# Kernel optimization log

Measured on AMD Instinct MI355X. Metric: run time of the kernel, lower is better.

## Reference

```python
import jax, jax.numpy as jnp
import numpy as np

B, N, H, IN, D, ET = 16, 128, 256, 4, 2, 2
E = N * (N - 1)
NRF = 4 * D + 1            # num_relative_features = 9 (2D)
NODE_F = IN + NRF + D      # 15
EDGE_F = 2 * NRF + IN + D  # 24
EPS = 1e-8


def _norm(v):
    return jnp.sqrt(jnp.sum(v * v, axis=-1, keepdims=True) + EPS)


def _rot(R, v):
    return jnp.einsum('...ij,...j->...i', R, v)


def _relfeat(dp, dv, R, dth):
    # rotation-invariant relative features in frame R: rotated rel pos/vel,
    # distances, polar angles, heading difference -> 2+2+1+1+1+1+1 = 9 dims
    rp = _rot(R, dp)
    rv = _rot(R, dv)
    ang = jnp.arctan2(rp[..., 1:2], rp[..., 0:1])
    vang = jnp.arctan2(rv[..., 1:2], rv[..., 0:1])
    return jnp.concatenate([rp, rv, _norm(dp), ang, _norm(dv), vang, dth], -1)


def _forward(inputs, hidden, edges, predicted_field,
             msg_fc1_w, msg_fc1_b, msg_fc2_w, msg_fc2_b,
             pm_fc1_w, pm_fc1_b, pm_fc2_w, pm_fc2_b,
             hidden_r_w, hidden_i_w, hidden_h_w,
             present_r_w, present_r_b, present_i_w, present_i_b,
             present_n_w, present_n_b,
             input_r_w, input_r_b, input_i_w, input_i_b, input_n_w, input_n_b,
             out_w1, out_b1, out_w2, out_b2, out_w3, out_b3,
             send, recv):
    # ---- recurrent message passing on hidden state ----
    pre_msg = jnp.concatenate([hidden[:, recv], hidden[:, send]], -1)  # [B,E,2H]
    all_msgs = jnp.zeros((B, E, H), pre_msg.dtype)
    for i in range(1, ET):  # skip_first_edge_type = True
        m = jnp.tanh(pre_msg @ msg_fc1_w[i].T + msg_fc1_b[i])
        m = jnp.tanh(m @ msg_fc2_w[i].T + msg_fc2_b[i])
        all_msgs = all_msgs + m * edges[:, :, i:i + 1]
    agg_msgs = jnp.zeros((B, N, H), all_msgs.dtype).at[:, recv].add(all_msgs) / (N - 1)

    # ---- localizer: per-node frame from velocity heading ----
    ext = jnp.concatenate([inputs, predicted_field], -1)  # [B,N,6]
    pos, vel, field = ext[..., :D], ext[..., D:2 * D], ext[..., 2 * D:]
    theta = jnp.arctan2(vel[..., 1], vel[..., 0])  # [B,N]
    c, s = jnp.cos(theta), jnp.sin(theta)
    R = jnp.stack([jnp.stack([c, s], -1), jnp.stack([-s, c], -1)], -2)  # [B,N,2,2]
    Rinv = jnp.swapaxes(R, -1, -2)

    loc_pos, loc_vel, loc_field = _rot(R, pos), _rot(R, vel), _rot(R, field)
    rel_self = _relfeat(pos, vel, R, theta[..., None])
    rel_feat = jnp.concatenate([rel_self, loc_pos, loc_vel, loc_field], -1)  # [B,N,15]

    dp = pos[:, send] - pos[:, recv]
    dv = vel[:, send] - vel[:, recv]
    dth = (theta[:, send] - theta[:, recv])[..., None]
    f1 = _relfeat(dp, dv, R[:, recv], dth)
    f2 = _relfeat(-dp, -dv, R[:, send], -dth)
    edge_attr = jnp.concatenate(
        [f1, f2, loc_pos[:, recv], loc_vel[:, recv], loc_field[:, recv]], -1)  # [B,E,24]

    # ---- present (observation) message passing ----
    present_msgs = jnp.zeros((B, E, H), edge_attr.dtype)
    for i in range(1, ET):
        m = jax.nn.relu(edge_attr @ pm_fc1_w[i].T + pm_fc1_b[i])
        m = jax.nn.relu(m @ pm_fc2_w[i].T + pm_fc2_b[i])
        present_msgs = present_msgs + m * edges[:, :, i:i + 1]
    present_agg = jnp.zeros((B, N, H), present_msgs.dtype).at[:, recv].add(present_msgs) / (N - 1)

    # ---- GRU-style gated update ----
    inp_r = rel_feat @ input_r_w.T + input_r_b + present_agg @ present_r_w.T + present_r_b
    inp_i = rel_feat @ input_i_w.T + input_i_b + present_agg @ present_i_w.T + present_i_b
    inp_n = rel_feat @ input_n_w.T + input_n_b + present_agg @ present_n_w.T + present_n_b
    r = jax.nn.sigmoid(inp_r + agg_msgs @ hidden_r_w.T)
    i_g = jax.nn.sigmoid(inp_i + agg_msgs @ hidden_i_w.T)
    n_g = jnp.tanh(inp_n + r * (agg_msgs @ hidden_h_w.T))
    hidden_new = (1.0 - i_g) * n_g + i_g * hidden

    # ---- output MLP + globalizer ----
    h1 = jax.nn.relu(hidden_new @ out_w1.T + out_b1)
    h2 = jax.nn.relu(h1 @ out_w2.T + out_b2)
    pred = h2 @ out_w3.T + out_b3  # [B,N,4]
    pred_global = jnp.concatenate(
        [_rot(Rinv, pred[..., :D]), _rot(Rinv, pred[..., D:2 * D])], -1)
    outputs = inputs + pred_global
    return outputs, hidden_new


def setup_inputs():
    key = jax.random.key(0)
    ks = iter(jax.random.split(key, 48))
    rn = lambda *s: jax.random.normal(next(ks), s, jnp.float32)
    w = lambda *s: rn(*s) * 0.05
    send, recv = np.where(~np.eye(N, dtype=bool))
    return dict(
        inputs=rn(B, N, IN), hidden=rn(B, N, H),
        edges=jax.random.uniform(next(ks), (B, E, ET), jnp.float32),
        predicted_field=rn(B, N, D),
        msg_fc1_w=w(ET, H, 2 * H), msg_fc1_b=w(ET, H),
        msg_fc2_w=w(ET, H, H), msg_fc2_b=w(ET, H),
        pm_fc1_w=w(ET, H, EDGE_F), pm_fc1_b=w(ET, H),
        pm_fc2_w=w(ET, H, H), pm_fc2_b=w(ET, H),
        hidden_r_w=w(H, H), hidden_i_w=w(H, H), hidden_h_w=w(H, H),
        present_r_w=w(H, H), present_r_b=w(H),
        present_i_w=w(H, H), present_i_b=w(H),
        present_n_w=w(H, H), present_n_b=w(H),
        input_r_w=w(H, NODE_F), input_r_b=w(H),
        input_i_w=w(H, NODE_F), input_i_b=w(H),
        input_n_w=w(H, NODE_F), input_n_b=w(H),
        out_w1=w(H, H), out_b1=w(H), out_w2=w(H, H), out_b2=w(H),
        out_w3=w(IN, H), out_b3=w(IN),
        send_edges=jnp.asarray(send, jnp.int32),
        recv_edges=jnp.asarray(recv, jnp.int32),
    )


def reference(inputs, hidden, edges, predicted_field,
              msg_fc1_w, msg_fc1_b, msg_fc2_w, msg_fc2_b,
              pm_fc1_w, pm_fc1_b, pm_fc2_w, pm_fc2_b,
              hidden_r_w, hidden_i_w, hidden_h_w,
              present_r_w, present_r_b, present_i_w, present_i_b,
              present_n_w, present_n_b,
              input_r_w, input_r_b, input_i_w, input_i_b, input_n_w, input_n_b,
              out_w1, out_b1, out_w2, out_b2, out_w3, out_b3,
              send_edges, recv_edges):
    return _forward(inputs, hidden, edges, predicted_field,
                    msg_fc1_w, msg_fc1_b, msg_fc2_w, msg_fc2_b,
                    pm_fc1_w, pm_fc1_b, pm_fc2_w, pm_fc2_b,
                    hidden_r_w, hidden_i_w, hidden_h_w,
                    present_r_w, present_r_b, present_i_w, present_i_b,
                    present_n_w, present_n_b,
                    input_r_w, input_r_b, input_i_w, input_i_b, input_n_w, input_n_b,
                    out_w1, out_b1, out_w2, out_b2, out_w3, out_b3,
                    send_edges, recv_edges)
```

## Files before the change

### kernel.cpp

```cpp
#include <hip/hip_runtime.h>
#include <math.h>

#define BB 16
#define NN 128
#define HH 256
#define EE (NN*(NN-1))

typedef unsigned short ushort_t;
typedef __attribute__((ext_vector_type(8))) short bf16x8;
typedef __attribute__((ext_vector_type(4))) float f32x4;

__device__ __forceinline__ ushort_t f2b(float f) {
  unsigned u = __builtin_bit_cast(unsigned, f);
  unsigned r = (u + 0x7fffu + ((u >> 16) & 1u)) >> 16;
  return (ushort_t)r;
}

__device__ __forceinline__ float fast_tanh(float x) {
  float xx = fminf(fmaxf(x, -15.f), 15.f);
  float e = __builtin_amdgcn_exp2f(xx * 2.8853900817779268f);
  return (e - 1.f) * __builtin_amdgcn_rcpf(e + 1.f);
}
__device__ __forceinline__ float fast_sigmoid(float x) {
  float xx = fminf(fmaxf(x, -30.f), 30.f);
  float e = __builtin_amdgcn_exp2f(-xx * 1.4426950408889634f);
  return __builtin_amdgcn_rcpf(1.f + e);
}

__global__ void k_node_geom(const float* __restrict__ inputs,
                            const float* __restrict__ pfield,
                            float* __restrict__ geom, float* __restrict__ relf) {
  int idx = blockIdx.x * blockDim.x + threadIdx.x;
  if (idx >= BB * NN) return;
  float px = inputs[idx*4+0], py = inputs[idx*4+1];
  float vx = inputs[idx*4+2], vy = inputs[idx*4+3];
  float fx = pfield[idx*2+0], fy = pfield[idx*2+1];
  float th = atan2f(vy, vx);
  float c = cosf(th), s = sinf(th);
  float lpx =  c*px + s*py, lpy = -s*px + c*py;
  float lvx =  c*vx + s*vy, lvy = -s*vx + c*vy;
  float lfx =  c*fx + s*fy, lfy = -s*fx + c*fy;
  float np_ = sqrtf(px*px + py*py + 1e-8f);
  float nv_ = sqrtf(vx*vx + vy*vy + 1e-8f);
  float ang  = atan2f(lpy, lpx);
  float vang = atan2f(lvy, lvx);
  float* g = geom + idx*16;
  g[0]=px; g[1]=py; g[2]=vx; g[3]=vy; g[4]=th; g[5]=c; g[6]=s;
  g[7]=lpx; g[8]=lpy; g[9]=lvx; g[10]=lvy; g[11]=lfx; g[12]=lfy;
  float* r = relf + idx*16;
  r[0]=lpx; r[1]=lpy; r[2]=lvx; r[3]=lvy; r[4]=np_; r[5]=ang; r[6]=nv_; r[7]=vang; r[8]=th;
  r[9]=lpx; r[10]=lpy; r[11]=lvx; r[12]=lvy; r[13]=lfx; r[14]=lfy;
}

__global__ void k_cvt(const float* __restrict__ w2, const float* __restrict__ pw2,
                      ushort_t* __restrict__ w2b, ushort_t* __restrict__ pw2b) {
  int idx = blockIdx.x * 256 + threadIdx.x;
  if (idx < HH*HH) w2b[idx] = f2b(w2[HH*HH + idx]);
  else { int k = idx - HH*HH; pw2b[k] = f2b(pw2[HH*HH + k]); }
}

__global__ __launch_bounds__(256) void k_hab(const float* __restrict__ hidden,
                                             const float* __restrict__ w1,
                                             const float* __restrict__ b1,
                                             float* __restrict__ Ha,
                                             float* __restrict__ Hb) {
  int n = blockIdx.x >> 1, half = blockIdx.x & 1;
  int tid = threadIdx.x;
  __shared__ float x[8][HH];
  for (int q = 0; q < 8; ++q) {
    int b = half*8 + q;
    x[q][tid] = hidden[(b*NN + n)*HH + tid];
  }
  __syncthreads();
  const float* wa = w1 + (HH*2*HH) + tid*(2*HH);
  const float* wb = wa + HH;
  float accA[8], accB[8];
  float bias = b1[HH + tid];
  #pragma unroll
  for (int q = 0; q < 8; ++q) { accA[q] = bias; accB[q] = 0.f; }
  for (int k = 0; k < HH; k += 4) {
    float4 a4 = *(const float4*)(wa + k);
    float4 b4 = *(const float4*)(wb + k);
    #pragma unroll
    for (int q = 0; q < 8; ++q) {
      float4 x4 = *(const float4*)(&x[q][k]);
      accA[q] += x4.x*a4.x + x4.y*a4.y + x4.z*a4.z + x4.w*a4.w;
      accB[q] += x4.x*b4.x + x4.y*b4.y + x4.z*b4.z + x4.w*b4.w;
    }
  }
  for (int q = 0; q < 8; ++q) {
    int b = half*8 + q;
    Ha[(b*NN + n)*HH + tid] = accA[q];
    Hb[(b*NN + n)*HH + tid] = accB[q];
  }
}

__global__ __launch_bounds__(256, 4) void k_edge(
    const float* __restrict__ Ha, const float* __restrict__ Hb,
    const float* __restrict__ geom, const float* __restrict__ edges,
    const ushort_t* __restrict__ w2b, const float* __restrict__ b2,
    const ushort_t* __restrict__ pw2b, const float* __restrict__ pb2,
    const float* __restrict__ pw1, const float* __restrict__ pb1,
    float* __restrict__ agg0, float* __restrict__ agg1,
    float* __restrict__ pagg0, float* __restrict__ pagg1) {
  int half = blockIdx.x & 1;
  int j = (blockIdx.x >> 1) & 127;
  int b = blockIdx.x >> 8;
  int tid = threadIdx.x;
  int lane = tid & 63;
  int wv = tid >> 6;
  int lrow = lane & 15, lk = lane >> 4;

  __shared__ __align__(16) unsigned char m1s[64*512];
  __shared__ float attrS[64][24];
  __shared__ float HajS[HH];
  __shared__ float wgtS[64];
  __shared__ float gjS[13];

  HajS[tid] = Ha[(b*NN + j)*HH + tid];
  if (tid < 13) gjS[tid] = geom[(b*NN + j)*16 + tid];
  __syncthreads();

  if (tid < 64) {
    int il = tid;
    int i = half*64 + il;
    const float* gi = geom + (b*NN + i)*16;
    float dpx = gi[0]-gjS[0], dpy = gi[1]-gjS[1];
    float dvx = gi[2]-gjS[2], dvy = gi[3]-gjS[3];
    float dth = gi[4]-gjS[4];
    float cj = gjS[5], sj = gjS[6];
    float ci = gi[5],  si = gi[6];
    float ndp = sqrtf(dpx*dpx + dpy*dpy + 1e-8f);
    float ndv = sqrtf(dvx*dvx + dvy*dvy + 1e-8f);
    float r1x =  cj*dpx + sj*dpy, r1y = -sj*dpx + cj*dpy;
    float v1x =  cj*dvx + sj*dvy, v1y = -sj*dvx + cj*dvy;
    attrS[il][0]=r1x; attrS[il][1]=r1y; attrS[il][2]=v1x; attrS[il][3]=v1y;
    attrS[il][4]=ndp; attrS[il][5]=atan2f(r1y, r1x);
    attrS[il][6]=ndv; attrS[il][7]=atan2f(v1y, v1x); attrS[il][8]=dth;
    float r2x = -(ci*dpx + si*dpy), r2y = si*dpx - ci*dpy;
    float v2x = -(ci*dvx + si*dvy), v2y = si*dvx - ci*dvy;
    attrS[il][9]=r2x; attrS[il][10]=r2y; attrS[il][11]=v2x; attrS[il][12]=v2y;
    attrS[il][13]=ndp; attrS[il][14]=atan2f(r2y, r2x);
    attrS[il][15]=ndv; attrS[il][16]=atan2f(v2y, v2x); attrS[il][17]=-dth;
    attrS[il][18]=gjS[7]; attrS[il][19]=gjS[8]; attrS[il][20]=gjS[9];
    attrS[il][21]=gjS[10]; attrS[il][22]=gjS[11]; attrS[il][23]=gjS[12];
    float w = 0.f;
    if (i != j) {
      int e = i*127 + (j < i ? j : j-1);
      w = edges[(b*EE + e)*2 + 1];
    }
    wgtS[il] = w;
  }

  {
    float haj = HajS[tid];
    const float* hb = Hb + (b*NN + half*64)*HH + tid;
    #pragma unroll
    for (int i0 = 0; i0 < 64; i0 += 8) {
      float v[8];
      #pragma unroll
      for (int u = 0; u < 8; ++u) v[u] = hb[(i0+u)*HH];
      #pragma unroll
      for (int u = 0; u < 8; ++u) {
        int row = i0 + u;
        *(ushort_t*)(m1s + row*512 + ((tid*2) ^ ((row&15)<<4))) =
            f2b(fast_tanh(haj + v[u]));
      }
    }
  }
  __syncthreads();

  f32x4 zero = {0.f, 0.f, 0.f, 0.f};

  {
    f32x4 acc[4][4];
    #pragma unroll
    for (int rt = 0; rt < 4; ++rt)
      #pragma unroll
      for (int nt = 0; nt < 4; ++nt) acc[rt][nt] = zero;
    for (int kk = 0; kk < 8; ++kk) {
      bf16x8 afr[4];
      #pragma unroll
      for (int rt = 0; rt < 4; ++rt) {
        int row = rt*16 + lrow;
        afr[rt] = *reinterpret_cast<const bf16x8*>(
            m1s + row*512 + ((kk*64 + lk*16) ^ ((row&15)<<4)));
      }
      #pragma unroll
      for (int nt = 0; nt < 4; ++nt) {
        int col = wv*64 + nt*16 + lrow;
        bf16x8 bfr = *reinterpret_cast<const bf16x8*>(w2b + col*HH + kk*32 + lk*8);
        #pragma unroll
        for (int rt = 0; rt < 4; ++rt)
          acc[rt][nt] = __builtin_amdgcn_mfma_f32_16x16x32_bf16(afr[rt], bfr, acc[rt][nt], 0, 0, 0);
      }
    }
    float* aggOut = half ? agg1 : agg0;
    #pragma unroll
    for (int nt = 0; nt < 4; ++nt) {
      int col = wv*64 + nt*16 + lrow;
      float bias = b2[col];
      float p = 0.f;
      #pragma unroll
      for (int rt = 0; rt < 4; ++rt)
        #pragma unroll
        for (int r = 0; r < 4; ++r) {
          int row = rt*16 + lk*4 + r;
          p += fast_tanh(acc[rt][nt][r] + bias) * wgtS[row];
        }
      p += __shfl_xor(p, 16);
      p += __shfl_xor(p, 32);
      if (lane < 16)
        aggOut[(b*NN + j)*HH + wv*64 + nt*16 + lane] = p * (1.0f/127.0f);
    }
  }
  __syncthreads();

  {
    float wrow[24];
    #pragma unroll
    for (int k = 0; k < 24; ++k) wrow[k] = pw1[tid*24 + k];
    float bias = pb1[tid];
    #pragma unroll 2
    for (int i = 0; i < 64; ++i) {
      float s = bias;
      #pragma unroll
      for (int k = 0; k < 24; k += 4) {
        float4 a4 = *(const float4*)(&attrS[i][k]);
        s += a4.x*wrow[k] + a4.y*wrow[k+1] + a4.z*wrow[k+2] + a4.w*wrow[k+3];
      }
      s = fmaxf(s, 0.f);
      *(ushort_t*)(m1s + i*512 + ((tid*2) ^ ((i&15)<<4))) = f2b(s);
    }
  }
  __syncthreads();

  {
    f32x4 acc[4][4];
    #pragma unroll
    for (int rt = 0; rt < 4; ++rt)
      #pragma unroll
      for (int nt = 0; nt < 4; ++nt) acc[rt][nt] = zero;
    for (int kk = 0; kk < 8; ++kk) {
      bf16x8 afr[4];
      #pragma unroll
      for (int rt = 0; rt < 4; ++rt) {
        int row = rt*16 + lrow;
        afr[rt] = *reinterpret_cast<const bf16x8*>(
            m1s + row*512 + ((kk*64 + lk*16) ^ ((row&15)<<4)));
      }
      #pragma unroll
      for (int nt = 0; nt < 4; ++nt) {
        int col = wv*64 + nt*16 + lrow;
        bf16x8 bfr = *reinterpret_cast<const bf16x8*>(pw2b + col*HH + kk*32 + lk*8);
        #pragma unroll
        for (int rt = 0; rt < 4; ++rt)
          acc[rt][nt] = __builtin_amdgcn_mfma_f32_16x16x32_bf16(afr[rt], bfr, acc[rt][nt], 0, 0, 0);
      }
    }
    float* paggOut = half ? pagg1 : pagg0;
    #pragma unroll
    for (int nt = 0; nt < 4; ++nt) {
      int col = wv*64 + nt*16 + lrow;
      float bias = pb2[col];
      float p = 0.f;
      #pragma unroll
      for (int rt = 0; rt < 4; ++rt)
        #pragma unroll
        for (int r = 0; r < 4; ++r) {
          int row = rt*16 + lk*4 + r;
          p += fmaxf(acc[rt][nt][r] + bias, 0.f) * wgtS[row];
        }
      p += __shfl_xor(p, 16);
      p += __shfl_xor(p, 32);
      if (lane < 16)
        paggOut[(b*NN + j)*HH + wv*64 + nt*16 + lane] = p * (1.0f/127.0f);
    }
  }
}

__global__ __launch_bounds__(256) void k_gru(
    const float* __restrict__ inputs, const float* __restrict__ hidden,
    const float* __restrict__ geom, const float* __restrict__ relf,
    const float* __restrict__ agg0, const float* __restrict__ agg1,
    const float* __restrict__ pagg0, const float* __restrict__ pagg1,
    const float* __restrict__ hr_w, const float* __restrict__ hi_w, const float* __restrict__ hh_w,
    const float* __restrict__ pr_w, const float* __restrict__ pr_b,
    const float* __restrict__ pi_w, const float* __restrict__ pi_b,
    const float* __restrict__ pn_w, const float* __restrict__ pn_b,
    const float* __restrict__ ir_w, const float* __restrict__ ir_b,
    const float* __restrict__ ii_w, const float* __restrict__ ii_b,
    const float* __restrict__ in_w, const float* __restrict__ in_b,
    const float* __restrict__ ow1, const float* __restrict__ ob1,
    const float* __restrict__ ow2, const float* __restrict__ ob2,
    const float* __restrict__ ow3, const float* __restrict__ ob3,
    float* __restrict__ out_o, float* __restrict__ out_h) {
  int n = blockIdx.x >> 1, half = blockIdx.x & 1;
  int tid = threadIdx.x;
  __shared__ float paS[8][HH], agS[8][HH], hS[8][HH], t0S[8][HH], t1S[8][HH];
  __shared__ float relS[8][16];
  __shared__ float predS[8][4];

  for (int q = 0; q < 8; ++q) {
    int b = half*8 + q;
    int base = (b*NN + n)*HH;
    paS[q][tid] = pagg0[base + tid] + pagg1[base + tid];
    agS[q][tid] = agg0[base + tid] + agg1[base + tid];
    hS[q][tid]  = hidden[base + tid];
  }
  if (tid < 128) {
    int q = tid >> 4, k = tid & 15;
    int b = half*8 + q;
    relS[q][k] = (k < 15) ? relf[(b*NN + n)*16 + k] : 0.f;
  }
  __syncthreads();

  int h = tid;
  float aR[8], aI[8], aN[8], aH[8];
  float br = ir_b[h] + pr_b[h];
  float bi = ii_b[h] + pi_b[h];
  float bn = in_b[h] + pn_b[h];
  #pragma unroll
  for (int q = 0; q < 8; ++q) { aR[q]=br; aI[q]=bi; aN[q]=bn; aH[q]=0.f; }

  for (int k = 0; k < 15; ++k) {
    float wr = ir_w[h*15+k], wi = ii_w[h*15+k], wn = in_w[h*15+k];
    #pragma unroll
    for (int q = 0; q < 8; ++q) {
      float x = relS[q][k];
      aR[q] += x*wr; aI[q] += x*wi; aN[q] += x*wn;
    }
  }
  for (int k = 0; k < HH; k += 4) {
    float4 wpr = *(const float4*)(pr_w + h*HH + k);
    float4 wpi = *(const float4*)(pi_w + h*HH + k);
    float4 wpn = *(const float4*)(pn_w + h*HH + k);
    float4 whr = *(const float4*)(hr_w + h*HH + k);
    float4 whi = *(const float4*)(hi_w + h*HH + k);
    float4 whh = *(const float4*)(hh_w + h*HH + k);
    #pragma unroll
    for (int q = 0; q < 8; ++q) {
      float4 xp = *(const float4*)(&paS[q][k]);
      float4 xa = *(const float4*)(&agS[q][k]);
      aR[q] += xp.x*wpr.x + xp.y*wpr.y + xp.z*wpr.z + xp.w*wpr.w
             + xa.x*whr.x + xa.y*whr.y + xa.z*whr.z + xa.w*whr.w;
      aI[q] += xp.x*wpi.x + xp.y*wpi.y + xp.z*wpi.z + xp.w*wpi.w
             + xa.x*whi.x + xa.y*whi.y + xa.z*whi.z + xa.w*whi.w;
      aN[q] += xp.x*wpn.x + xp.y*wpn.y + xp.z*wpn.z + xp.w*wpn.w;
      aH[q] += xa.x*whh.x + xa.y*whh.y + xa.z*whh.z + xa.w*whh.w;
    }
  }
  #pragma unroll
  for (int q = 0; q < 8; ++q) {
    int b = half*8 + q;
    float r  = fast_sigmoid(aR[q]);
    float ig = fast_sigmoid(aI[q]);
    float ng = fast_tanh(aN[q] + r*aH[q]);
    float hn = (1.f - ig)*ng + ig*hS[q][h];
    out_h[(b*NN + n)*HH + h] = hn;
    t0S[q][h] = hn;
  }
  __syncthreads();

  {
    float a1[8];
    float bias = ob1[h];
    #pragma unroll
    for (int q = 0; q < 8; ++q) a1[q] = bias;
    for (int k = 0; k < HH; k += 4) {
      float4 w = *(const float4*)(ow1 + h*HH + k);
      #pragma unroll
      for (int q = 0; q < 8; ++q) {
        float4 x = *(const float4*)(&t0S[q][k]);
        a1[q] += x.x*w.x + x.y*w.y + x.z*w.z + x.w*w.w;
      }
    }
    __syncthreads();
    #pragma unroll
    for (int q = 0; q < 8; ++q) t1S[q][h] = fmaxf(a1[q], 0.f);
  }
  __syncthreads();

  {
    float a2[8];
    float bias = ob2[h];
    #pragma unroll
    for (int q = 0; q < 8; ++q) a2[q] = bias;
    for (int k = 0; k < HH; k += 4) {
      float4 w = *(const float4*)(ow2 + h*HH + k);
      #pragma unroll
      for (int q = 0; q < 8; ++q) {
        float4 x = *(const float4*)(&t1S[q][k]);
        a2[q] += x.x*w.x + x.y*w.y + x.z*w.z + x.w*w.w;
      }
    }
    __syncthreads();
    #pragma unroll
    for (int q = 0; q < 8; ++q) t0S[q][h] = fmaxf(a2[q], 0.f);
  }
  __syncthreads();

  if (tid < 32) {
    int o = tid >> 3, q = tid & 7;
    float acc = ob3[o];
    for (int k = 0; k < HH; ++k) acc += t0S[q][k]*ow3[o*HH + k];
    predS[q][o] = acc;
  }
  __syncthreads();
  if (tid < 8) {
    int q = tid;
    int b = half*8 + q;
    const float* g = geom + (b*NN + n)*16;
    float c = g[5], s = g[6];
    float p0 = predS[q][0], p1 = predS[q][1], p2 = predS[q][2], p3 = predS[q][3];
    int base = (b*NN + n)*4;
    out_o[base+0] = inputs[base+0] + (c*p0 - s*p1);
    out_o[base+1] = inputs[base+1] + (s*p0 + c*p1);
    out_o[base+2] = inputs[base+2] + (c*p2 - s*p3);
    out_o[base+3] = inputs[base+3] + (s*p2 + c*p3);
  }
}

extern "C" void kernel_launch(void* const* d_in, const int* in_sizes, int n_in,
                              void* d_out, int out_size, void* d_ws, size_t ws_size,
                              hipStream_t stream) {
  const float* inputs    = (const float*)d_in[0];
  const float* hidden    = (const float*)d_in[1];
  const float* edges     = (const float*)d_in[2];
  const float* pfield    = (const float*)d_in[3];
  const float* msg_fc1_w = (const float*)d_in[4];
  const float* msg_fc1_b = (const float*)d_in[5];
  const float* msg_fc2_w = (const float*)d_in[6];
  const float* msg_fc2_b = (const float*)d_in[7];
  const float* pm_fc1_w  = (const float*)d_in[8];
  const float* pm_fc1_b  = (const float*)d_in[9];
  const float* pm_fc2_w  = (const float*)d_in[10];
  const float* pm_fc2_b  = (const float*)d_in[11];
  const float* hr_w = (const float*)d_in[12];
  const float* hi_w = (const float*)d_in[13];
  const float* hh_w = (const float*)d_in[14];
  const float* pr_w = (const float*)d_in[15];
  const float* pr_b = (const float*)d_in[16];
  const float* pi_w = (const float*)d_in[17];
  const float* pi_b = (const float*)d_in[18];
  const float* pn_w = (const float*)d_in[19];
  const float* pn_b = (const float*)d_in[20];
  const float* ir_w = (const float*)d_in[21];
  const float* ir_b = (const float*)d_in[22];
  const float* ii_w = (const float*)d_in[23];
  const float* ii_b = (const float*)d_in[24];
  const float* in_w = (const float*)d_in[25];
  const float* in_b = (const float*)d_in[26];
  const float* ow1  = (const float*)d_in[27];
  const float* ob1  = (const float*)d_in[28];
  const float* ow2  = (const float*)d_in[29];
  const float* ob2  = (const float*)d_in[30];
  const float* ow3  = (const float*)d_in[31];
  const float* ob3  = (const float*)d_in[32];

  float* ws   = (float*)d_ws;
  float* geom = ws;
  float* relf = geom + 32768;
  float* Ha   = relf + 32768;
  float* Hb   = Ha   + 524288;
  float* agg0 = Hb   + 524288;
  float* agg1 = agg0 + 524288;
  float* pagg0= agg1 + 524288;
  float* pagg1= pagg0+ 524288;
  ushort_t* w2b  = (ushort_t*)(pagg1 + 524288);
  ushort_t* pw2b = w2b + HH*HH;

  float* out_o = (float*)d_out;
  float* out_h = out_o + BB*NN*4;

  k_node_geom<<<dim3(8), dim3(256), 0, stream>>>(inputs, pfield, geom, relf);
  k_cvt<<<dim3(512), dim3(256), 0, stream>>>(msg_fc2_w, pm_fc2_w, w2b, pw2b);
  k_hab<<<dim3(256), dim3(256), 0, stream>>>(hidden, msg_fc1_w, msg_fc1_b, Ha, Hb);
  k_edge<<<dim3(BB*NN*2), dim3(256), 0, stream>>>(Ha, Hb, geom, edges,
      w2b, msg_fc2_b + HH, pw2b, pm_fc2_b + HH,
      pm_fc1_w + HH*24, pm_fc1_b + HH, agg0, agg1, pagg0, pagg1);
  k_gru<<<dim3(256), dim3(256), 0, stream>>>(inputs, hidden, geom, relf,
      agg0, agg1, pagg0, pagg1,
      hr_w, hi_w, hh_w, pr_w, pr_b, pi_w, pi_b, pn_w, pn_b,
      ir_w, ir_b, ii_w, ii_b, in_w, in_b,
      ow1, ob1, ow2, ob2, ow3, ob3, out_o, out_h);
}
```

Before: 483.6 us.

## Use bf16 MFMA for edge pm_fc1 layer and double grid for hab/gru

The per-edge 24-input pm_fc1 layer, formerly scalar FP32 dot products per thread, now runs as one bf16 MFMA step. Edge attributes are packed as zero-padded bf16 rows in swizzled shared memory, and the layer weights are converted to bf16 and padded to K=32 in the conversion kernel. Separately, k_hab and k_gru process 4 batches per block instead of 8, doubling their grid to 512 blocks for more parallelism at the cost of rereading weights more often. Rounding the attributes to bf16 adds precision loss in the edge-feature MLP input.

```diff
diff --git a/kernel.cpp b/kernel.cpp
--- a/kernel.cpp
+++ b/kernel.cpp
@@ -53,10 +53,20 @@
 }
 
 __global__ void k_cvt(const float* __restrict__ w2, const float* __restrict__ pw2,
-                      ushort_t* __restrict__ w2b, ushort_t* __restrict__ pw2b) {
+                      const float* __restrict__ pw1,
+                      ushort_t* __restrict__ w2b, ushort_t* __restrict__ pw2b,
+                      ushort_t* __restrict__ pw1b) {
   int idx = blockIdx.x * 256 + threadIdx.x;
-  if (idx < HH*HH) w2b[idx] = f2b(w2[HH*HH + idx]);
-  else { int k = idx - HH*HH; pw2b[k] = f2b(pw2[HH*HH + k]); }
+  if (idx < HH*HH) {
+    w2b[idx] = f2b(w2[HH*HH + idx]);
+  } else if (idx < 2*HH*HH) {
+    int k = idx - HH*HH;
+    pw2b[k] = f2b(pw2[HH*HH + k]);
+  } else if (idx < 2*HH*HH + HH*32) {
+    int k = idx - 2*HH*HH;
+    int col = k >> 5, kk = k & 31;
+    pw1b[k] = (kk < 24) ? f2b(pw1[col*24 + kk]) : (ushort_t)0;
+  }
 }
 
 __global__ __launch_bounds__(256) void k_hab(const float* __restrict__ hidden,
@@ -64,32 +74,32 @@
                                              const float* __restrict__ b1,
                                              float* __restrict__ Ha,
                                              float* __restrict__ Hb) {
-  int n = blockIdx.x >> 1, half = blockIdx.x & 1;
+  int n = blockIdx.x >> 2, qtr = blockIdx.x & 3;
   int tid = threadIdx.x;
-  __shared__ float x[8][HH];
-  for (int q = 0; q < 8; ++q) {
-    int b = half*8 + q;
+  __shared__ float x[4][HH];
+  for (int q = 0; q < 4; ++q) {
+    int b = qtr*4 + q;
     x[q][tid] = hidden[(b*NN + n)*HH + tid];
   }
   __syncthreads();
   const float* wa = w1 + (HH*2*HH) + tid*(2*HH);
   const float* wb = wa + HH;
-  float accA[8], accB[8];
+  float accA[4], accB[4];
   float bias = b1[HH + tid];
   #pragma unroll
-  for (int q = 0; q < 8; ++q) { accA[q] = bias; accB[q] = 0.f; }
+  for (int q = 0; q < 4; ++q) { accA[q] = bias; accB[q] = 0.f; }
   for (int k = 0; k < HH; k += 4) {
     float4 a4 = *(const float4*)(wa + k);
     float4 b4 = *(const float4*)(wb + k);
     #pragma unroll
-    for (int q = 0; q < 8; ++q) {
+    for (int q = 0; q < 4; ++q) {
       float4 x4 = *(const float4*)(&x[q][k]);
       accA[q] += x4.x*a4.x + x4.y*a4.y + x4.z*a4.z + x4.w*a4.w;
       accB[q] += x4.x*b4.x + x4.y*b4.y + x4.z*b4.z + x4.w*b4.w;
     }
   }
-  for (int q = 0; q < 8; ++q) {
-    int b = half*8 + q;
+  for (int q = 0; q < 4; ++q) {
+    int b = qtr*4 + q;
     Ha[(b*NN + n)*HH + tid] = accA[q];
     Hb[(b*NN + n)*HH + tid] = accB[q];
   }
@@ -100,7 +110,7 @@
     const float* __restrict__ geom, const float* __restrict__ edges,
     const ushort_t* __restrict__ w2b, const float* __restrict__ b2,
     const ushort_t* __restrict__ pw2b, const float* __restrict__ pb2,
-    const float* __restrict__ pw1, const float* __restrict__ pb1,
+    const ushort_t* __restrict__ pw1b, const float* __restrict__ pb1,
     float* __restrict__ agg0, float* __restrict__ agg1,
     float* __restrict__ pagg0, float* __restrict__ pagg1) {
   int half = blockIdx.x & 1;
@@ -112,7 +122,7 @@
   int lrow = lane & 15, lk = lane >> 4;
 
   __shared__ __align__(16) unsigned char m1s[64*512];
-  __shared__ float attrS[64][24];
+  __shared__ __align__(16) unsigned char attrB[64*64];
   __shared__ float HajS[HH];
   __shared__ float wgtS[64];
   __shared__ float gjS[13];
@@ -134,16 +144,27 @@
     float ndv = sqrtf(dvx*dvx + dvy*dvy + 1e-8f);
     float r1x =  cj*dpx + sj*dpy, r1y = -sj*dpx + cj*dpy;
     float v1x =  cj*dvx + sj*dvy, v1y = -sj*dvx + cj*dvy;
-    attrS[il][0]=r1x; attrS[il][1]=r1y; attrS[il][2]=v1x; attrS[il][3]=v1y;
-    attrS[il][4]=ndp; attrS[il][5]=atan2f(r1y, r1x);
-    attrS[il][6]=ndv; attrS[il][7]=atan2f(v1y, v1x); attrS[il][8]=dth;
     float r2x = -(ci*dpx + si*dpy), r2y = si*dpx - ci*dpy;
     float v2x = -(ci*dvx + si*dvy), v2y = si*dvx - ci*dvy;
-    attrS[il][9]=r2x; attrS[il][10]=r2y; attrS[il][11]=v2x; attrS[il][12]=v2y;
-    attrS[il][13]=ndp; attrS[il][14]=atan2f(r2y, r2x);
-    attrS[il][15]=ndv; attrS[il][16]=atan2f(v2y, v2x); attrS[il][17]=-dth;
-    attrS[il][18]=gjS[7]; attrS[il][19]=gjS[8]; attrS[il][20]=gjS[9];
-    attrS[il][21]=gjS[10]; attrS[il][22]=gjS[11]; attrS[il][23]=gjS[12];
+    float f[24];
+    f[0]=r1x; f[1]=r1y; f[2]=v1x; f[3]=v1y;
+    f[4]=ndp; f[5]=atan2f(r1y, r1x);
+    f[6]=ndv; f[7]=atan2f(v1y, v1x); f[8]=dth;
+    f[9]=r2x; f[10]=r2y; f[11]=v2x; f[12]=v2y;
+    f[13]=ndp; f[14]=atan2f(r2y, r2x);
+    f[15]=ndv; f[16]=atan2f(v2y, v2x); f[17]=-dth;
+    f[18]=gjS[7]; f[19]=gjS[8]; f[20]=gjS[9];
+    f[21]=gjS[10]; f[22]=gjS[11]; f[23]=gjS[12];
+    #pragma unroll
+    for (int kb = 0; kb < 4; ++kb) {
+      bf16x8 v;
+      #pragma unroll
+      for (int e = 0; e < 8; ++e) {
+        int k = kb*8 + e;
+        v[e] = (k < 24) ? (short)f2b(f[k]) : (short)0;
+      }
+      *reinterpret_cast<bf16x8*>(attrB + il*64 + ((kb*16) ^ ((il&3)<<4))) = v;
+    }
     float w = 0.f;
     if (i != j) {
       int e = i*127 + (j < i ? j : j-1);
@@ -217,20 +238,38 @@
   __syncthreads();
 
   {
-    float wrow[24];
-    #pragma unroll
-    for (int k = 0; k < 24; ++k) wrow[k] = pw1[tid*24 + k];
-    float bias = pb1[tid];
-    #pragma unroll 2
-    for (int i = 0; i < 64; ++i) {
-      float s = bias;
-      #pragma unroll
-      for (int k = 0; k < 24; k += 4) {
-        float4 a4 = *(const float4*)(&attrS[i][k]);
-        s += a4.x*wrow[k] + a4.y*wrow[k+1] + a4.z*wrow[k+2] + a4.w*wrow[k+3];
-      }
-      s = fmaxf(s, 0.f);
-      *(ushort_t*)(m1s + i*512 + ((tid*2) ^ ((i&15)<<4))) = f2b(s);
+    f32x4 acc[4][4];
+    #pragma unroll
+    for (int rt = 0; rt < 4; ++rt)
+      #pragma unroll
+      for (int nt = 0; nt < 4; ++nt) acc[rt][nt] = zero;
+    bf16x8 afr[4];
+    #pragma unroll
+    for (int rt = 0; rt < 4; ++rt) {
+      int row = rt*16 + lrow;
+      afr[rt] = *reinterpret_cast<const bf16x8*>(
+          attrB + row*64 + ((lk*16) ^ ((lrow&3)<<4)));
+    }
+    #pragma unroll
+    for (int nt = 0; nt < 4; ++nt) {
+      int col = wv*64 + nt*16 + lrow;
+      bf16x8 bfr = *reinterpret_cast<const bf16x8*>(pw1b + col*32 + lk*8);
+      #pragma unroll
+      for (int rt = 0; rt < 4; ++rt)
+        acc[rt][nt] = __builtin_amdgcn_mfma_f32_16x16x32_bf16(afr[rt], bfr, acc[rt][nt], 0, 0, 0);
+    }
+    #pragma unroll
+    for (int nt = 0; nt < 4; ++nt) {
+      int col = wv*64 + nt*16 + lrow;
+      float bias = pb1[col];
+      #pragma unroll
+      for (int rt = 0; rt < 4; ++rt)
+        #pragma unroll
+        for (int r = 0; r < 4; ++r) {
+          int row = rt*16 + lk*4 + r;
+          *(ushort_t*)(m1s + row*512 + ((col*2) ^ ((row&15)<<4))) =
+              f2b(fmaxf(acc[rt][nt][r] + bias, 0.f));
+        }
     }
   }
   __syncthreads();
@@ -295,38 +334,38 @@
     const float* __restrict__ ow2, const float* __restrict__ ob2,
     const float* __restrict__ ow3, const float* __restrict__ ob3,
     float* __restrict__ out_o, float* __restrict__ out_h) {
-  int n = blockIdx.x >> 1, half = blockIdx.x & 1;
+  int n = blockIdx.x >> 2, qtr = blockIdx.x & 3;
   int tid = threadIdx.x;
-  __shared__ float paS[8][HH], agS[8][HH], hS[8][HH], t0S[8][HH], t1S[8][HH];
-  __shared__ float relS[8][16];
-  __shared__ float predS[8][4];
-
-  for (int q = 0; q < 8; ++q) {
-    int b = half*8 + q;
+  __shared__ float paS[4][HH], agS[4][HH], hS[4][HH], t0S[4][HH], t1S[4][HH];
+  __shared__ float relS[4][16];
+  __shared__ float predS[4][4];
+
+  for (int q = 0; q < 4; ++q) {
+    int b = qtr*4 + q;
     int base = (b*NN + n)*HH;
     paS[q][tid] = pagg0[base + tid] + pagg1[base + tid];
     agS[q][tid] = agg0[base + tid] + agg1[base + tid];
     hS[q][tid]  = hidden[base + tid];
   }
-  if (tid < 128) {
+  if (tid < 64) {
     int q = tid >> 4, k = tid & 15;
-    int b = half*8 + q;
+    int b = qtr*4 + q;
     relS[q][k] = (k < 15) ? relf[(b*NN + n)*16 + k] : 0.f;
   }
   __syncthreads();
 
   int h = tid;
-  float aR[8], aI[8], aN[8], aH[8];
+  float aR[4], aI[4], aN[4], aH[4];
   float br = ir_b[h] + pr_b[h];
   float bi = ii_b[h] + pi_b[h];
   float bn = in_b[h] + pn_b[h];
   #pragma unroll
-  for (int q = 0; q < 8; ++q) { aR[q]=br; aI[q]=bi; aN[q]=bn; aH[q]=0.f; }
+  for (int q = 0; q < 4; ++q) { aR[q]=br; aI[q]=bi; aN[q]=bn; aH[q]=0.f; }
 
   for (int k = 0; k < 15; ++k) {
     float wr = ir_w[h*15+k], wi = ii_w[h*15+k], wn = in_w[h*15+k];
     #pragma unroll
-    for (int q = 0; q < 8; ++q) {
+    for (int q = 0; q < 4; ++q) {
       float x = relS[q][k];
       aR[q] += x*wr; aI[q] += x*wi; aN[q] += x*wn;
     }
@@ -339,7 +378,7 @@
     float4 whi = *(const float4*)(hi_w + h*HH + k);
     float4 whh = *(const float4*)(hh_w + h*HH + k);
     #pragma unroll
-    for (int q = 0; q < 8; ++q) {
+    for (int q = 0; q < 4; ++q) {
       float4 xp = *(const float4*)(&paS[q][k]);
       float4 xa = *(const float4*)(&agS[q][k]);
       aR[q] += xp.x*wpr.x + xp.y*wpr.y + xp.z*wpr.z + xp.w*wpr.w
@@ -351,8 +390,8 @@
     }
   }
   #pragma unroll
-  for (int q = 0; q < 8; ++q) {
-    int b = half*8 + q;
+  for (int q = 0; q < 4; ++q) {
+    int b = qtr*4 + q;
     float r  = fast_sigmoid(aR[q]);
     float ig = fast_sigmoid(aI[q]);
     float ng = fast_tanh(aN[q] + r*aH[q]);
@@ -363,53 +402,53 @@
   __syncthreads();
 
   {
-    float a1[8];
+    float a1[4];
     float bias = ob1[h];
     #pragma unroll
-    for (int q = 0; q < 8; ++q) a1[q] = bias;
+    for (int q = 0; q < 4; ++q) a1[q] = bias;
     for (int k = 0; k < HH; k += 4) {
       float4 w = *(const float4*)(ow1 + h*HH + k);
       #pragma unroll
-      for (int q = 0; q < 8; ++q) {
+      for (int q = 0; q < 4; ++q) {
         float4 x = *(const float4*)(&t0S[q][k]);
         a1[q] += x.x*w.x + x.y*w.y + x.z*w.z + x.w*w.w;
       }
     }
     __syncthreads();
     #pragma unroll
-    for (int q = 0; q < 8; ++q) t1S[q][h] = fmaxf(a1[q], 0.f);
+    for (int q = 0; q < 4; ++q) t1S[q][h] = fmaxf(a1[q], 0.f);
   }
   __syncthreads();
 
   {
-    float a2[8];
+    float a2[4];
     float bias = ob2[h];
     #pragma unroll
-    for (int q = 0; q < 8; ++q) a2[q] = bias;
+    for (int q = 0; q < 4; ++q) a2[q] = bias;
     for (int k = 0; k < HH; k += 4) {
       float4 w = *(const float4*)(ow2 + h*HH + k);
       #pragma unroll
-      for (int q = 0; q < 8; ++q) {
+      for (int q = 0; q < 4; ++q) {
         float4 x = *(const float4*)(&t1S[q][k]);
         a2[q] += x.x*w.x + x.y*w.y + x.z*w.z + x.w*w.w;
       }
     }
     __syncthreads();
     #pragma unroll
-    for (int q = 0; q < 8; ++q) t0S[q][h] = fmaxf(a2[q], 0.f);
-  }
-  __syncthreads();
-
-  if (tid < 32) {
-    int o = tid >> 3, q = tid & 7;
+    for (int q = 0; q < 4; ++q) t0S[q][h] = fmaxf(a2[q], 0.f);
+  }
+  __syncthreads();
+
+  if (tid < 16) {
+    int o = tid >> 2, q = tid & 3;
     float acc = ob3[o];
     for (int k = 0; k < HH; ++k) acc += t0S[q][k]*ow3[o*HH + k];
     predS[q][o] = acc;
   }
   __syncthreads();
-  if (tid < 8) {
+  if (tid < 4) {
     int q = tid;
-    int b = half*8 + q;
+    int b = qtr*4 + q;
     const float* g = geom + (b*NN + n)*16;
     float c = g[5], s = g[6];
     float p0 = predS[q][0], p1 = predS[q][1], p2 = predS[q][2], p3 = predS[q][3];
@@ -469,17 +508,19 @@
   float* pagg1= pagg0+ 524288;
   ushort_t* w2b  = (ushort_t*)(pagg1 + 524288);
   ushort_t* pw2b = w2b + HH*HH;
+  ushort_t* pw1b = pw2b + HH*HH;
 
   float* out_o = (float*)d_out;
   float* out_h = out_o + BB*NN*4;
 
   k_node_geom<<<dim3(8), dim3(256), 0, stream>>>(inputs, pfield, geom, relf);
-  k_cvt<<<dim3(512), dim3(256), 0, stream>>>(msg_fc2_w, pm_fc2_w, w2b, pw2b);
-  k_hab<<<dim3(256), dim3(256), 0, stream>>>(hidden, msg_fc1_w, msg_fc1_b, Ha, Hb);
+  k_cvt<<<dim3(544), dim3(256), 0, stream>>>(msg_fc2_w, pm_fc2_w,
+      pm_fc1_w + HH*24, w2b, pw2b, pw1b);
+  k_hab<<<dim3(512), dim3(256), 0, stream>>>(hidden, msg_fc1_w, msg_fc1_b, Ha, Hb);
   k_edge<<<dim3(BB*NN*2), dim3(256), 0, stream>>>(Ha, Hb, geom, edges,
       w2b, msg_fc2_b + HH, pw2b, pm_fc2_b + HH,
-      pm_fc1_w + HH*24, pm_fc1_b + HH, agg0, agg1, pagg0, pagg1);
-  k_gru<<<dim3(256), dim3(256), 0, stream>>>(inputs, hidden, geom, relf,
+      pw1b, pm_fc1_b + HH, agg0, agg1, pagg0, pagg1);
+  k_gru<<<dim3(512), dim3(256), 0, stream>>>(inputs, hidden, geom, relf,
       agg0, agg1, pagg0, pagg1,
       hr_w, hi_w, hh_w, pr_w, pr_b, pi_w, pi_b, pn_w, pn_b,
       ir_w, ir_b, ii_w, ii_b, in_w, in_b,
```

Result: slower. 528.5 us (+9.3%).
